# Kernel optimization log

Hardware: AMD Instinct MI355X
Metric: run time of the kernel (lower is better)

## Reference

```python
import jax, jax.numpy as jnp
import numpy as np

N, E, IN_DIM, HID, OUT, H = 50000, 800000, 128, 96, 96, 4
C1, C2 = HID // H, OUT // H
EPS = 1e-5

def _lin(key, out_f, in_f):
    kw, kb = jax.random.split(key)
    s = 1.0 / np.sqrt(in_f)
    W = jax.random.uniform(kw, (out_f, in_f), jnp.float32, -s, s)
    b = jax.random.uniform(kb, (out_f,), jnp.float32, -s, s)
    return W, b

def setup_inputs() -> dict:
    key = jax.random.key(0)
    ks = jax.random.split(key, 16)
    x = jax.random.normal(ks[0], (N, IN_DIM), jnp.float32)
    edge_index = jax.random.randint(ks[1], (2, E), 0, N, jnp.int64)
    Wq1, bq1 = _lin(ks[2], HID, IN_DIM)
    Wk1, bk1 = _lin(ks[3], HID, IN_DIM)
    Wv1, bv1 = _lin(ks[4], HID, IN_DIM)
    Ws1, bs1 = _lin(ks[5], HID, IN_DIM)
    Wb1 = _lin(ks[6], 1, 3 * HID)[0]
    Wq2, bq2 = _lin(ks[7], OUT, HID)
    Wk2, bk2 = _lin(ks[8], OUT, HID)
    Wv2, bv2 = _lin(ks[9], OUT, HID)
    Ws2, bs2 = _lin(ks[10], OUT, HID)
    Wb2 = _lin(ks[11], 1, 3 * OUT)[0]
    gamma = jnp.ones((OUT,), jnp.float32)
    beta = jnp.zeros((OUT,), jnp.float32)
    return dict(x=x, edge_index=edge_index, Wq1=Wq1, bq1=bq1, Wk1=Wk1, bk1=bk1,
                Wv1=Wv1, bv1=bv1, Ws1=Ws1, bs1=bs1, Wb1=Wb1,
                Wq2=Wq2, bq2=bq2, Wk2=Wk2, bk2=bk2, Wv2=Wv2, bv2=bv2,
                Ws2=Ws2, bs2=bs2, Wb2=Wb2, gamma=gamma, beta=beta)

def transformer_conv(x, src, dst, Wq, bq, Wk, bk, Wv, bv, Ws, bs, Wb, heads, ch):
    n = x.shape[0]
    q = (x @ Wq.T + bq).reshape(n, heads, ch)
    k = (x @ Wk.T + bk).reshape(n, heads, ch)
    v = (x @ Wv.T + bv).reshape(n, heads, ch)
    # per-edge attention logits [E, H]
    alpha = jnp.einsum('ehc,ehc->eh', q[dst], k[src]) / jnp.sqrt(jnp.float32(ch))
    amax = jax.ops.segment_max(alpha, dst, num_segments=n)
    a = jnp.exp(alpha - amax[dst])
    denom = jax.ops.segment_sum(a, dst, num_segments=n)
    a = a / denom[dst]
    msg = v[src] * a[:, :, None]                       # [E, H, C]
    out = jax.ops.segment_sum(msg, dst, num_segments=n).reshape(n, heads * ch)
    x_r = x @ Ws.T + bs                                # root/skip transform
    g = jax.nn.sigmoid(jnp.concatenate([out, x_r, out - x_r], -1) @ Wb.T)
    return g * x_r + (1.0 - g) * out

def reference(x, edge_index, Wq1, bq1, Wk1, bk1, Wv1, bv1, Ws1, bs1, Wb1,
              Wq2, bq2, Wk2, bk2, Wv2, bv2, Ws2, bs2, Wb2, gamma, beta):
    src, dst = edge_index[0], edge_index[1]
    h = transformer_conv(x, src, dst, Wq1, bq1, Wk1, bk1, Wv1, bv1, Ws1, bs1, Wb1, H, C1)
    h = jax.nn.gelu(h, approximate=False)
    h = transformer_conv(h, src, dst, Wq2, bq2, Wk2, bk2, Wv2, bv2, Ws2, bs2, Wb2, H, C2)
    mu = jnp.mean(h, axis=-1, keepdims=True)
    var = jnp.mean(jnp.square(h - mu), axis=-1, keepdims=True)
    return (h - mu) / jnp.sqrt(var + EPS) * gamma + beta
```

## Files before the change

kernel.cpp:

```cpp
#include <hip/hip_runtime.h>
#include <hip/hip_bf16.h>
#include <hip/hip_fp16.h>
#include <math.h>

constexpr int NN = 50000;
constexpr int EE = 800000;
constexpr int SCAN_NB = (NN + 255) / 256;
constexpr int HISTB   = (EE + 255) / 256;
constexpr int GEMMB4  = (NN + 15) / 16;

typedef short v8s __attribute__((ext_vector_type(8)));
typedef float v4f __attribute__((ext_vector_type(4)));

__device__ __forceinline__ short f2b(float f){
  __hip_bfloat16 h = __float2bfloat16(f);
  return *reinterpret_cast<short*>(&h);
}
__device__ __forceinline__ __half2 u2h2(unsigned int u){
  union { unsigned int u; __half2 h; } c; c.u = u; return c.h;
}

__global__ __launch_bounds__(256) void histpack_kernel(
    const int* __restrict__ ei, int* __restrict__ degC, int* __restrict__ epos,
    const float* __restrict__ Wq1, const float* __restrict__ bq1,
    const float* __restrict__ Wk1, const float* __restrict__ bk1,
    const float* __restrict__ Wv1, const float* __restrict__ bv1,
    const float* __restrict__ Ws1, const float* __restrict__ bs1,
    const float* __restrict__ Wq2, const float* __restrict__ bq2,
    const float* __restrict__ Wk2, const float* __restrict__ bk2,
    const float* __restrict__ Wv2, const float* __restrict__ bv2,
    const float* __restrict__ Ws2, const float* __restrict__ bs2,
    const float* __restrict__ Wb1, const float* __restrict__ Wb2,
    short* __restrict__ Wcat1, float* __restrict__ bcat1,
    short* __restrict__ Wcat2, float* __restrict__ bcat2,
    float* __restrict__ wa1, float* __restrict__ wc1,
    float* __restrict__ wa2, float* __restrict__ wc2){
  int b = blockIdx.x;
  if (b < HISTB){
    int e = b * 256 + threadIdx.x;
    if (e < EE){
      int dst = ei[EE + e];
      int c = b & 7;
      int old = atomicAdd(&degC[c * NN + dst], 1);
      epos[e] = (c << 28) | old;
    }
  } else if (b < HISTB + 768){
    int c = b - HISTB;
    int layer = c / 384, cc = c % 384;
    int which = cc / 96, r = cc % 96;
    const float *Wsel, *bsel;
    int K; short* Wd; float* bd;
    if (layer == 0){
      Wsel = which == 0 ? Wq1 : which == 1 ? Wk1 : which == 2 ? Wv1 : Ws1;
      bsel = which == 0 ? bq1 : which == 1 ? bk1 : which == 2 ? bv1 : bs1;
      K = 128; Wd = Wcat1; bd = bcat1;
    } else {
      Wsel = which == 0 ? Wq2 : which == 1 ? Wk2 : which == 2 ? Wv2 : Ws2;
      bsel = which == 0 ? bq2 : which == 1 ? bk2 : which == 2 ? bv2 : bs2;
      K = 96; Wd = Wcat2; bd = bcat2;
    }
    for (int k = threadIdx.x; k < K; k += blockDim.x)
      Wd[(size_t)cc * K + k] = f2b(Wsel[(size_t)r * K + k]);
    if (threadIdx.x == 0) bd[cc] = bsel[r];
  } else {
    int t = threadIdx.x;
    if (t < 96){
      wa1[t] = Wb1[t] + Wb1[192 + t];
      wc1[t] = Wb1[96 + t] - Wb1[192 + t];
    } else if (t < 192){
      int f = t - 96;
      wa2[f] = Wb2[f] + Wb2[192 + f];
      wc2[f] = Wb2[96 + f] - Wb2[192 + f];
    }
  }
}

__global__ __launch_bounds__(256) void partial_sum_kernel(const int* __restrict__ degC,
                                                          int* __restrict__ psum){
  int b = blockIdx.x, tid = threadIdx.x, lane = tid & 63, wv = tid >> 6;
  int i = b * 256 + tid;
  int v = 0;
  if (i < NN){
    #pragma unroll
    for (int c = 0; c < 8; c++) v += degC[c * NN + i];
  }
  #pragma unroll
  for (int m = 1; m < 64; m <<= 1) v += __shfl_xor(v, m);
  __shared__ int ws[4];
  if (lane == 0) ws[wv] = v;
  __syncthreads();
  if (tid == 0) psum[b] = ws[0] + ws[1] + ws[2] + ws[3];
}

__global__ __launch_bounds__(256) void scan_partials_kernel(int* __restrict__ psum){
  int tid = threadIdx.x, lane = tid & 63, wv = tid >> 6;
  int own = (tid < SCAN_NB) ? psum[tid] : 0;
  int v = own;
  #pragma unroll
  for (int off = 1; off < 64; off <<= 1){
    int t = __shfl_up(v, off);
    if (lane >= off) v += t;
  }
  __shared__ int ws[4];
  if (lane == 63) ws[wv] = v;
  __syncthreads();
  int add = 0;
  #pragma unroll
  for (int w = 0; w < 4; w++) if (w < wv) add += ws[w];
  if (tid < SCAN_NB) psum[tid] = v + add - own;
}

__global__ __launch_bounds__(256) void final_scan_kernel(const int* __restrict__ degC,
                                                         const int* __restrict__ psum,
                                                         int* __restrict__ row_ptr,
                                                         int* __restrict__ base8){
  int b = blockIdx.x, tid = threadIdx.x, lane = tid & 63, wv = tid >> 6;
  int i = b * 256 + tid;
  int dc[8];
  int d = 0;
  if (i < NN){
    #pragma unroll
    for (int c = 0; c < 8; c++){ dc[c] = degC[c * NN + i]; d += dc[c]; }
  } else {
    #pragma unroll
    for (int c = 0; c < 8; c++) dc[c] = 0;
  }
  int v = d;
  #pragma unroll
  for (int off = 1; off < 64; off <<= 1){
    int t = __shfl_up(v, off);
    if (lane >= off) v += t;
  }
  __shared__ int ws[4];
  if (lane == 63) ws[wv] = v;
  __syncthreads();
  int add = psum[b];
  #pragma unroll
  for (int w = 0; w < 4; w++) if (w < wv) add += ws[w];
  if (i < NN){
    int start = add + v - d;
    row_ptr[i + 1] = add + v;
    int run = start;
    #pragma unroll
    for (int c = 0; c < 8; c++){
      base8[(size_t)i * 8 + c] = run;
      run += dc[c];
    }
  }
  if (i == 0) row_ptr[0] = 0;
}

__global__ void fill_kernel(const int* __restrict__ ei, const int* __restrict__ epos,
                            const int* __restrict__ base8,
                            unsigned short* __restrict__ col_src){
  int e = blockIdx.x * blockDim.x + threadIdx.x;
  if (e < EE){
    int src = ei[e], dst = ei[EE + e];
    unsigned int u = (unsigned int)epos[e];
    int c = u >> 28, cnt = u & 0x0FFFFFFF;
    int pos = base8[(size_t)dst * 8 + c] + cnt;
    col_src[pos] = (unsigned short)src;
  }
}

template<int K, bool AF32>
__global__ __launch_bounds__(256) void gemm_kernel(const void* __restrict__ Ain,
                                                   const short* __restrict__ Wcat,
                                                   const float* __restrict__ bcat,
                                                   __half* __restrict__ qsh,
                                                   __half* __restrict__ kvb, int M){
  constexpr int NK = K / 32;
  const int tid = threadIdx.x;
  const int lane = tid & 63;
  const int wave_id = blockIdx.x * 4 + (tid >> 6);
  const int tile = wave_id >> 2;
  const int quarter = wave_id & 3;
  if (tile * 16 >= M) return;
  const int rt = tile * 16;
  const int fr = lane & 15, fk = lane >> 4;
  const int arow = rt + fr;

  v8s a[NK];
  if constexpr (AF32){
    const float* A = (const float*)Ain;
    #pragma unroll
    for (int ks = 0; ks < NK; ks++){
      const float* p = A + (size_t)arow * K + ks * 32 + fk * 8;
      float4 a0 = *(const float4*)p;
      float4 a1 = *(const float4*)(p + 4);
      v8s o;
      o[0] = f2b(a0.x); o[1] = f2b(a0.y); o[2] = f2b(a0.z); o[3] = f2b(a0.w);
      o[4] = f2b(a1.x); o[5] = f2b(a1.y); o[6] = f2b(a1.z); o[7] = f2b(a1.w);
      a[ks] = o;
    }
  } else {
    const short* A = (const short*)Ain;
    #pragma unroll
    for (int ks = 0; ks < NK; ks++)
      a[ks] = *(const v8s*)(A + (size_t)arow * K + ks * 32 + fk * 8);
  }

  #pragma unroll
  for (int pp = 0; pp < 6; pp++){
    const int p = quarter * 6 + pp;
    const int c0 = p * 16;
    const int gcol = c0 + fr;
    v4f acc = (v4f){0.f, 0.f, 0.f, 0.f};
    #pragma unroll
    for (int ks = 0; ks < NK; ks++){
      v8s b = *(const v8s*)(Wcat + (size_t)gcol * K + ks * 32 + fk * 8);
      acc = __builtin_amdgcn_mfma_f32_16x16x32_bf16(a[ks], b, acc, 0, 0, 0);
    }
    const float bias = bcat[gcol];
    if (c0 < 96){
      #pragma unroll
      for (int r = 0; r < 4; r++)
        qsh[(size_t)(rt + fk * 4 + r) * 192 + gcol] = __float2half(acc[r] + bias);
    } else if (c0 < 192){
      #pragma unroll
      for (int r = 0; r < 4; r++)
        kvb[(size_t)(rt + fk * 4 + r) * 192 + (gcol - 96)] = __float2half(acc[r] + bias);
    } else if (c0 < 288){
      #pragma unroll
      for (int r = 0; r < 4; r++)
        kvb[(size_t)(rt + fk * 4 + r) * 192 + 96 + (gcol - 192)] = __float2half(acc[r] + bias);
    } else {
      #pragma unroll
      for (int r = 0; r < 4; r++)
        qsh[(size_t)(rt + fk * 4 + r) * 192 + 96 + (gcol - 288)] = __float2half(acc[r] + bias);
    }
  }
}

__global__ __launch_bounds__(256) void attn_kernel(
    const __half* __restrict__ qs, const __half* __restrict__ kv,
    const int* __restrict__ row_ptr, const unsigned short* __restrict__ col_src,
    const float* __restrict__ wa, const float* __restrict__ wc,
    const float* __restrict__ gamma, const float* __restrict__ beta,
    float* __restrict__ outp, short* __restrict__ h1b, int mode){
  const int lane = threadIdx.x & 63;
  const int wid  = threadIdx.x >> 6;
  const int n = blockIdx.x * 4 + wid;
  if (n >= NN) return;
  const int h_a = lane & 3;
  const int g_a = lane >> 2;
  const int l_v = lane & 15;
  const int vg  = lane >> 4;
  const int h_v = l_v >> 2;
  const char* kvc = (const char*)kv;
  const char* qsc = (const char*)qs;

  __half2 qh[12];
  {
    const uint4* qp = (const uint4*)(qsc + (size_t)n * 384 + h_a * 48);
    uint4 a0 = qp[0], a1 = qp[1], a2 = qp[2];
    qh[0] = u2h2(a0.x); qh[1] = u2h2(a0.y); qh[2]  = u2h2(a0.z); qh[3]  = u2h2(a0.w);
    qh[4] = u2h2(a1.x); qh[5] = u2h2(a1.y); qh[6]  = u2h2(a1.z); qh[7]  = u2h2(a1.w);
    qh[8] = u2h2(a2.x); qh[9] = u2h2(a2.y); qh[10] = u2h2(a2.z); qh[11] = u2h2(a2.w);
  }
  const int rs = row_ptr[n], re = row_ptr[n + 1];
  float m = -INFINITY, s = 0.f;
  float acc[6] = {0.f, 0.f, 0.f, 0.f, 0.f, 0.f};

  for (int cb = rs; cb < re; cb += 16){
    const int cn = re - cb;
    int srcv = col_src[cb + min(g_a, cn - 1)];
    int sb[4];
    #pragma unroll
    for (int st = 0; st < 4; st++)
      sb[st] = __shfl(srcv, 4 * min(st * 4 + vg, cn - 1));
    unsigned int vd[4][3];
    #pragma unroll
    for (int st = 0; st < 4; st++){
      const unsigned int* vp =
        (const unsigned int*)(kvc + (size_t)sb[st] * 384 + 192 + 12 * l_v);
      vd[st][0] = vp[0]; vd[st][1] = vp[1]; vd[st][2] = vp[2];
    }
    const uint4* kp = (const uint4*)(kvc + (size_t)srcv * 384 + h_a * 48);
    uint4 u0 = kp[0], u1 = kp[1], u2 = kp[2];
    __half2 d0 = __floats2half2_rn(0.f, 0.f), d1 = d0;
    d0 = __hfma2(qh[0],  u2h2(u0.x), d0); d1 = __hfma2(qh[1],  u2h2(u0.y), d1);
    d0 = __hfma2(qh[2],  u2h2(u0.z), d0); d1 = __hfma2(qh[3],  u2h2(u0.w), d1);
    d0 = __hfma2(qh[4],  u2h2(u1.x), d0); d1 = __hfma2(qh[5],  u2h2(u1.y), d1);
    d0 = __hfma2(qh[6],  u2h2(u1.z), d0); d1 = __hfma2(qh[7],  u2h2(u1.w), d1);
    d0 = __hfma2(qh[8],  u2h2(u2.x), d0); d1 = __hfma2(qh[9],  u2h2(u2.y), d1);
    d0 = __hfma2(qh[10], u2h2(u2.z), d0); d1 = __hfma2(qh[11], u2h2(u2.w), d1);
    float dot = __low2float(d0) + __high2float(d0) + __low2float(d1) + __high2float(d1);
    float al = (g_a < cn) ? dot * 0.2041241452319315f : -INFINITY;

    float cm = al;
    cm = fmaxf(cm, __shfl_xor(cm, 4));
    cm = fmaxf(cm, __shfl_xor(cm, 8));
    cm = fmaxf(cm, __shfl_xor(cm, 16));
    cm = fmaxf(cm, __shfl_xor(cm, 32));
    float nm = fmaxf(m, cm);
    float r  = __expf(m - nm);
    float e  = __expf(al - nm);
    float cs = e;
    cs += __shfl_xor(cs, 4);
    cs += __shfl_xor(cs, 8);
    cs += __shfl_xor(cs, 16);
    cs += __shfl_xor(cs, 32);
    s = s * r + cs;
    m = nm;

    float rv = __shfl(r, h_v);
    __half2 ch0 = __floats2half2_rn(0.f, 0.f), ch1 = ch0, ch2 = ch0;
    #pragma unroll
    for (int st = 0; st < 4; st++){
      int eidx = st * 4 + vg;
      float w = __shfl(e, 4 * min(eidx, cn - 1) + h_v);
      if (eidx >= cn) w = 0.f;
      __half2 w2 = __float2half2_rn(w);
      ch0 = __hfma2(w2, u2h2(vd[st][0]), ch0);
      ch1 = __hfma2(w2, u2h2(vd[st][1]), ch1);
      ch2 = __hfma2(w2, u2h2(vd[st][2]), ch2);
    }
    acc[0] = fmaf(acc[0], rv, __low2float(ch0));
    acc[1] = fmaf(acc[1], rv, __high2float(ch0));
    acc[2] = fmaf(acc[2], rv, __low2float(ch1));
    acc[3] = fmaf(acc[3], rv, __high2float(ch1));
    acc[4] = fmaf(acc[4], rv, __low2float(ch2));
    acc[5] = fmaf(acc[5], rv, __high2float(ch2));
  }

  #pragma unroll
  for (int i = 0; i < 6; i++){
    acc[i] += __shfl_xor(acc[i], 16);
    acc[i] += __shfl_xor(acc[i], 32);
  }
  float sv  = __shfl(s, h_v);
  float inv = (re > rs) ? 1.0f / sv : 0.f;
  float o[6], xr[6];
  #pragma unroll
  for (int i = 0; i < 6; i++) o[i] = acc[i] * inv;
  {
    const unsigned int* xp = (const unsigned int*)(qsc + (size_t)n * 384 + 192 + 12 * l_v);
    unsigned int x0 = xp[0], x1 = xp[1], x2 = xp[2];
    xr[0] = __low2float(u2h2(x0)); xr[1] = __high2float(u2h2(x0));
    xr[2] = __low2float(u2h2(x1)); xr[3] = __high2float(u2h2(x1));
    xr[4] = __low2float(u2h2(x2)); xr[5] = __high2float(u2h2(x2));
  }

  float p = 0.f;
  #pragma unroll
  for (int i = 0; i < 6; i++){
    int f = 6 * l_v + i;
    p = fmaf(o[i], wa[f], p);
    p = fmaf(xr[i], wc[f], p);
  }
  p += __shfl_xor(p, 1);
  p += __shfl_xor(p, 2);
  p += __shfl_xor(p, 4);
  p += __shfl_xor(p, 8);
  float g = 1.0f / (1.0f + __expf(-p));
  float y[6];
  #pragma unroll
  for (int i = 0; i < 6; i++) y[i] = fmaf(g, xr[i] - o[i], o[i]);

  if (mode == 0){
    #pragma unroll
    for (int i = 0; i < 6; i++)
      y[i] = 0.5f * y[i] * (1.0f + erff(y[i] * 0.7071067811865475f));
    if (vg == 0){
      short* op = h1b + (size_t)n * 96 + 6 * l_v;
      #pragma unroll
      for (int i = 0; i < 6; i++) op[i] = f2b(y[i]);
    }
  } else {
    float ssum = y[0] + y[1] + y[2] + y[3] + y[4] + y[5];
    ssum += __shfl_xor(ssum, 1);
    ssum += __shfl_xor(ssum, 2);
    ssum += __shfl_xor(ssum, 4);
    ssum += __shfl_xor(ssum, 8);
    float mu = ssum * (1.0f / 96.0f);
    float vsum = 0.f;
    #pragma unroll
    for (int i = 0; i < 6; i++){ float d = y[i] - mu; vsum += d * d; }
    vsum += __shfl_xor(vsum, 1);
    vsum += __shfl_xor(vsum, 2);
    vsum += __shfl_xor(vsum, 4);
    vsum += __shfl_xor(vsum, 8);
    float invs = rsqrtf(vsum * (1.0f / 96.0f) + 1e-5f);
    if (vg == 0){
      float* op = outp + (size_t)n * 96 + 6 * l_v;
      #pragma unroll
      for (int i = 0; i < 6; i++){
        int f = 6 * l_v + i;
        op[i] = (y[i] - mu) * invs * gamma[f] + beta[f];
      }
    }
  }
}

extern "C" void kernel_launch(void* const* d_in, const int* in_sizes, int n_in,
                              void* d_out, int out_size, void* d_ws, size_t ws_size,
                              hipStream_t stream){
  const float* x    = (const float*)d_in[0];
  const int*   ei   = (const int*)d_in[1];
  const float* Wq1  = (const float*)d_in[2];
  const float* bq1  = (const float*)d_in[3];
  const float* Wk1  = (const float*)d_in[4];
  const float* bk1  = (const float*)d_in[5];
  const float* Wv1  = (const float*)d_in[6];
  const float* bv1  = (const float*)d_in[7];
  const float* Ws1  = (const float*)d_in[8];
  const float* bs1  = (const float*)d_in[9];
  const float* Wb1  = (const float*)d_in[10];
  const float* Wq2  = (const float*)d_in[11];
  const float* bq2  = (const float*)d_in[12];
  const float* Wk2  = (const float*)d_in[13];
  const float* bk2  = (const float*)d_in[14];
  const float* Wv2  = (const float*)d_in[15];
  const float* bv2  = (const float*)d_in[16];
  const float* Ws2  = (const float*)d_in[17];
  const float* bs2  = (const float*)d_in[18];
  const float* Wb2  = (const float*)d_in[19];
  const float* gamma = (const float*)d_in[20];
  const float* beta  = (const float*)d_in[21];
  float* out = (float*)d_out;

  char* ws = (char*)d_ws;
  size_t off = 0;
  auto take = [&](size_t b) -> void* {
    void* p = ws + off;
    off += (b + 255) & ~(size_t)255;
    return p;
  };
  __half* qs           = (__half*)take((size_t)NN * 192 * 2);
  __half* kvb          = (__half*)take((size_t)NN * 192 * 2);
  short* h1b           = (short*)take((size_t)NN * 96 * 2);
  short* Wcat1         = (short*)take((size_t)384 * 128 * 2);
  short* Wcat2         = (short*)take((size_t)384 * 96 * 2);
  float* bcat1         = (float*)take(384 * 4);
  float* bcat2         = (float*)take(384 * 4);
  float* wa1           = (float*)take(96 * 4);
  float* wc1           = (float*)take(96 * 4);
  float* wa2           = (float*)take(96 * 4);
  float* wc2           = (float*)take(96 * 4);
  int* degC            = (int*)take((size_t)8 * NN * 4);
  int* epos            = (int*)take((size_t)EE * 4);
  int* base8           = (int*)take((size_t)NN * 8 * 4);
  int* row_ptr         = (int*)take((size_t)(NN + 1) * 4);
  unsigned short* col_src = (unsigned short*)take((size_t)EE * 2);
  int* psum            = (int*)take((size_t)SCAN_NB * 4);

  hipMemsetAsync(degC, 0, (size_t)8 * NN * 4, stream);
  histpack_kernel<<<HISTB + 768 + 1, 256, 0, stream>>>(
      ei, degC, epos,
      Wq1, bq1, Wk1, bk1, Wv1, bv1, Ws1, bs1,
      Wq2, bq2, Wk2, bk2, Wv2, bv2, Ws2, bs2,
      Wb1, Wb2, Wcat1, bcat1, Wcat2, bcat2, wa1, wc1, wa2, wc2);
  partial_sum_kernel<<<SCAN_NB, 256, 0, stream>>>(degC, psum);
  scan_partials_kernel<<<1, 256, 0, stream>>>(psum);
  final_scan_kernel<<<SCAN_NB, 256, 0, stream>>>(degC, psum, row_ptr, base8);
  fill_kernel<<<(EE + 255) / 256, 256, 0, stream>>>(ei, epos, base8, col_src);

  gemm_kernel<128, true><<<GEMMB4, 256, 0, stream>>>(x, Wcat1, bcat1, qs, kvb, NN);
  attn_kernel<<<(NN + 3) / 4, 256, 0, stream>>>(qs, kvb, row_ptr, col_src,
                                                wa1, wc1, nullptr, nullptr,
                                                nullptr, h1b, 0);
  gemm_kernel<96, false><<<GEMMB4, 256, 0, stream>>>(h1b, Wcat2, bcat2, qs, kvb, NN);
  attn_kernel<<<(NN + 3) / 4, 256, 0, stream>>>(qs, kvb, row_ptr, col_src,
                                                wa2, wc2, gamma, beta,
                                                out, nullptr, 1);
}
```

Before: 241.4 us.

## Fuse edge histogram with layer-1 projection GEMM in one launch

The weight packing moves into its own small kernel. The edge-degree histogram and the layer-1 QKV/skip GEMM now share one kernel, with block ranges assigned to each task. The aim is for the atomic-heavy histogram and the MFMA GEMM to overlap on the GPU and to save one launch, which requires the packed weights to be ready before the fused launch. The packing kernel now runs alone and serially ahead of the fused kernel, which adds a dependency step in exchange.

```diff
diff --git a/kernel.cpp b/kernel.cpp
--- a/kernel.cpp
+++ b/kernel.cpp
@@ -20,8 +20,7 @@
   union { unsigned int u; __half2 h; } c; c.u = u; return c.h;
 }
 
-__global__ __launch_bounds__(256) void histpack_kernel(
-    const int* __restrict__ ei, int* __restrict__ degC, int* __restrict__ epos,
+__global__ __launch_bounds__(128) void pack_kernel(
     const float* __restrict__ Wq1, const float* __restrict__ bq1,
     const float* __restrict__ Wk1, const float* __restrict__ bk1,
     const float* __restrict__ Wv1, const float* __restrict__ bv1,
@@ -35,17 +34,8 @@
     short* __restrict__ Wcat2, float* __restrict__ bcat2,
     float* __restrict__ wa1, float* __restrict__ wc1,
     float* __restrict__ wa2, float* __restrict__ wc2){
-  int b = blockIdx.x;
-  if (b < HISTB){
-    int e = b * 256 + threadIdx.x;
-    if (e < EE){
-      int dst = ei[EE + e];
-      int c = b & 7;
-      int old = atomicAdd(&degC[c * NN + dst], 1);
-      epos[e] = (c << 28) | old;
-    }
-  } else if (b < HISTB + 768){
-    int c = b - HISTB;
+  int c = blockIdx.x;
+  if (c < 768){
     int layer = c / 384, cc = c % 384;
     int which = cc / 96, r = cc % 96;
     const float *Wsel, *bsel;
@@ -67,12 +57,107 @@
     if (t < 96){
       wa1[t] = Wb1[t] + Wb1[192 + t];
       wc1[t] = Wb1[96 + t] - Wb1[192 + t];
-    } else if (t < 192){
-      int f = t - 96;
-      wa2[f] = Wb2[f] + Wb2[192 + f];
-      wc2[f] = Wb2[96 + f] - Wb2[192 + f];
-    }
-  }
+      wa2[t] = Wb2[t] + Wb2[192 + t];
+      wc2[t] = Wb2[96 + t] - Wb2[192 + t];
+    }
+  }
+}
+
+template<int K, bool AF32>
+__device__ __forceinline__ void gemm_body(int wave_id, const void* __restrict__ Ain,
+                                          const short* __restrict__ Wcat,
+                                          const float* __restrict__ bcat,
+                                          __half* __restrict__ qsh,
+                                          __half* __restrict__ kvb, int M){
+  constexpr int NK = K / 32;
+  const int lane = threadIdx.x & 63;
+  const int tile = wave_id >> 2;
+  const int quarter = wave_id & 3;
+  if (tile * 16 >= M) return;
+  const int rt = tile * 16;
+  const int fr = lane & 15, fk = lane >> 4;
+  const int arow = rt + fr;
+
+  v8s a[NK];
+  if constexpr (AF32){
+    const float* A = (const float*)Ain;
+    #pragma unroll
+    for (int ks = 0; ks < NK; ks++){
+      const float* p = A + (size_t)arow * K + ks * 32 + fk * 8;
+      float4 a0 = *(const float4*)p;
+      float4 a1 = *(const float4*)(p + 4);
+      v8s o;
+      o[0] = f2b(a0.x); o[1] = f2b(a0.y); o[2] = f2b(a0.z); o[3] = f2b(a0.w);
+      o[4] = f2b(a1.x); o[5] = f2b(a1.y); o[6] = f2b(a1.z); o[7] = f2b(a1.w);
+      a[ks] = o;
+    }
+  } else {
+    const short* A = (const short*)Ain;
+    #pragma unroll
+    for (int ks = 0; ks < NK; ks++)
+      a[ks] = *(const v8s*)(A + (size_t)arow * K + ks * 32 + fk * 8);
+  }
+
+  #pragma unroll
+  for (int pp = 0; pp < 6; pp++){
+    const int p = quarter * 6 + pp;
+    const int c0 = p * 16;
+    const int gcol = c0 + fr;
+    v4f acc = (v4f){0.f, 0.f, 0.f, 0.f};
+    #pragma unroll
+    for (int ks = 0; ks < NK; ks++){
+      v8s b = *(const v8s*)(Wcat + (size_t)gcol * K + ks * 32 + fk * 8);
+      acc = __builtin_amdgcn_mfma_f32_16x16x32_bf16(a[ks], b, acc, 0, 0, 0);
+    }
+    const float bias = bcat[gcol];
+    if (c0 < 96){
+      #pragma unroll
+      for (int r = 0; r < 4; r++)
+        qsh[(size_t)(rt + fk * 4 + r) * 192 + gcol] = __float2half(acc[r] + bias);
+    } else if (c0 < 192){
+      #pragma unroll
+      for (int r = 0; r < 4; r++)
+        kvb[(size_t)(rt + fk * 4 + r) * 192 + (gcol - 96)] = __float2half(acc[r] + bias);
+    } else if (c0 < 288){
+      #pragma unroll
+      for (int r = 0; r < 4; r++)
+        kvb[(size_t)(rt + fk * 4 + r) * 192 + 96 + (gcol - 192)] = __float2half(acc[r] + bias);
+    } else {
+      #pragma unroll
+      for (int r = 0; r < 4; r++)
+        qsh[(size_t)(rt + fk * 4 + r) * 192 + 96 + (gcol - 288)] = __float2half(acc[r] + bias);
+    }
+  }
+}
+
+__global__ __launch_bounds__(256) void histgemm_kernel(
+    const int* __restrict__ ei, int* __restrict__ degC, int* __restrict__ epos,
+    const void* __restrict__ Ain, const short* __restrict__ Wcat,
+    const float* __restrict__ bcat, __half* __restrict__ qsh,
+    __half* __restrict__ kvb, int M){
+  int b = blockIdx.x;
+  if (b < HISTB){
+    int e = b * 256 + threadIdx.x;
+    if (e < EE){
+      int dst = ei[EE + e];
+      int c = b & 7;
+      int old = atomicAdd(&degC[c * NN + dst], 1);
+      epos[e] = (c << 28) | old;
+    }
+  } else {
+    int wave_id = (b - HISTB) * 4 + (threadIdx.x >> 6);
+    gemm_body<128, true>(wave_id, Ain, Wcat, bcat, qsh, kvb, M);
+  }
+}
+
+template<int K, bool AF32>
+__global__ __launch_bounds__(256) void gemm_kernel(const void* __restrict__ Ain,
+                                                   const short* __restrict__ Wcat,
+                                                   const float* __restrict__ bcat,
+                                                   __half* __restrict__ qsh,
+                                                   __half* __restrict__ kvb, int M){
+  int wave_id = blockIdx.x * 4 + (threadIdx.x >> 6);
+  gemm_body<K, AF32>(wave_id, Ain, Wcat, bcat, qsh, kvb, M);
 }
 
 __global__ __launch_bounds__(256) void partial_sum_kernel(const int* __restrict__ degC,
@@ -160,75 +245,6 @@
     int c = u >> 28, cnt = u & 0x0FFFFFFF;
     int pos = base8[(size_t)dst * 8 + c] + cnt;
     col_src[pos] = (unsigned short)src;
-  }
-}
-
-template<int K, bool AF32>
-__global__ __launch_bounds__(256) void gemm_kernel(const void* __restrict__ Ain,
-                                                   const short* __restrict__ Wcat,
-                                                   const float* __restrict__ bcat,
-                                                   __half* __restrict__ qsh,
-                                                   __half* __restrict__ kvb, int M){
-  constexpr int NK = K / 32;
-  const int tid = threadIdx.x;
-  const int lane = tid & 63;
-  const int wave_id = blockIdx.x * 4 + (tid >> 6);
-  const int tile = wave_id >> 2;
-  const int quarter = wave_id & 3;
-  if (tile * 16 >= M) return;
-  const int rt = tile * 16;
-  const int fr = lane & 15, fk = lane >> 4;
-  const int arow = rt + fr;
-
-  v8s a[NK];
-  if constexpr (AF32){
-    const float* A = (const float*)Ain;
-    #pragma unroll
-    for (int ks = 0; ks < NK; ks++){
-      const float* p = A + (size_t)arow * K + ks * 32 + fk * 8;
-      float4 a0 = *(const float4*)p;
-      float4 a1 = *(const float4*)(p + 4);
-      v8s o;
-      o[0] = f2b(a0.x); o[1] = f2b(a0.y); o[2] = f2b(a0.z); o[3] = f2b(a0.w);
-      o[4] = f2b(a1.x); o[5] = f2b(a1.y); o[6] = f2b(a1.z); o[7] = f2b(a1.w);
-      a[ks] = o;
-    }
-  } else {
-    const short* A = (const short*)Ain;
-    #pragma unroll
-    for (int ks = 0; ks < NK; ks++)
-      a[ks] = *(const v8s*)(A + (size_t)arow * K + ks * 32 + fk * 8);
-  }
-
-  #pragma unroll
-  for (int pp = 0; pp < 6; pp++){
-    const int p = quarter * 6 + pp;
-    const int c0 = p * 16;
-    const int gcol = c0 + fr;
-    v4f acc = (v4f){0.f, 0.f, 0.f, 0.f};
-    #pragma unroll
-    for (int ks = 0; ks < NK; ks++){
-      v8s b = *(const v8s*)(Wcat + (size_t)gcol * K + ks * 32 + fk * 8);
-      acc = __builtin_amdgcn_mfma_f32_16x16x32_bf16(a[ks], b, acc, 0, 0, 0);
-    }
-    const float bias = bcat[gcol];
-    if (c0 < 96){
-      #pragma unroll
-      for (int r = 0; r < 4; r++)
-        qsh[(size_t)(rt + fk * 4 + r) * 192 + gcol] = __float2half(acc[r] + bias);
-    } else if (c0 < 192){
-      #pragma unroll
-      for (int r = 0; r < 4; r++)
-        kvb[(size_t)(rt + fk * 4 + r) * 192 + (gcol - 96)] = __float2half(acc[r] + bias);
-    } else if (c0 < 288){
-      #pragma unroll
-      for (int r = 0; r < 4; r++)
-        kvb[(size_t)(rt + fk * 4 + r) * 192 + 96 + (gcol - 192)] = __float2half(acc[r] + bias);
-    } else {
-      #pragma unroll
-      for (int r = 0; r < 4; r++)
-        qsh[(size_t)(rt + fk * 4 + r) * 192 + 96 + (gcol - 288)] = __float2half(acc[r] + bias);
-    }
   }
 }
 
@@ -446,17 +462,17 @@
   int* psum            = (int*)take((size_t)SCAN_NB * 4);
 
   hipMemsetAsync(degC, 0, (size_t)8 * NN * 4, stream);
-  histpack_kernel<<<HISTB + 768 + 1, 256, 0, stream>>>(
-      ei, degC, epos,
+  pack_kernel<<<769, 128, 0, stream>>>(
       Wq1, bq1, Wk1, bk1, Wv1, bv1, Ws1, bs1,
       Wq2, bq2, Wk2, bk2, Wv2, bv2, Ws2, bs2,
       Wb1, Wb2, Wcat1, bcat1, Wcat2, bcat2, wa1, wc1, wa2, wc2);
+  histgemm_kernel<<<HISTB + GEMMB4, 256, 0, stream>>>(
+      ei, degC, epos, x, Wcat1, bcat1, qs, kvb, NN);
   partial_sum_kernel<<<SCAN_NB, 256, 0, stream>>>(degC, psum);
   scan_partials_kernel<<<1, 256, 0, stream>>>(psum);
   final_scan_kernel<<<SCAN_NB, 256, 0, stream>>>(degC, psum, row_ptr, base8);
   fill_kernel<<<(EE + 255) / 256, 256, 0, stream>>>(ei, epos, base8, col_src);
 
-  gemm_kernel<128, true><<<GEMMB4, 256, 0, stream>>>(x, Wcat1, bcat1, qs, kvb, NN);
   attn_kernel<<<(NN + 3) / 4, 256, 0, stream>>>(qs, kvb, row_ptr, col_src,
                                                 wa1, wc1, nullptr, nullptr,
                                                 nullptr, h1b, 0);
```

Measured after the change: 240.7 us. About the same (-0.3%).
